# Kernel tuning notes

Measured on AMD Instinct MI355X. Metric: run time of the kernel, lower is better.

## Reference

```python
import jax, jax.numpy as jnp
import numpy as np

T = 4096          # total packed tokens
E = 1024          # embed_dim
H = 16            # num heads
D = E // H        # head_dim
NEG = -1e30       # masked score (fp32-safe; every row has >=1 valid key)


def setup_inputs() -> dict:
    key = jax.random.key(0)
    ks = jax.random.split(key, 10)
    hidden_states = jax.random.normal(ks[0], (T, E), dtype=jnp.float32)
    # ragged segment boundaries (8 segments, varying lengths, packed to T)
    cu_seqlens = jnp.array([0, 400, 900, 1500, 2100, 2600, 3100, 3700, T], dtype=jnp.int32)
    s = 0.02
    Wq = jax.random.normal(ks[1], (E, E), dtype=jnp.float32) * s
    bq = jax.random.normal(ks[2], (E,), dtype=jnp.float32) * s
    Wk = jax.random.normal(ks[3], (E, E), dtype=jnp.float32) * s
    bk = jax.random.normal(ks[4], (E,), dtype=jnp.float32) * s
    Wv = jax.random.normal(ks[5], (E, E), dtype=jnp.float32) * s
    bv = jax.random.normal(ks[6], (E,), dtype=jnp.float32) * s
    Wo = jax.random.normal(ks[7], (E, E), dtype=jnp.float32) * s
    bo = jax.random.normal(ks[8], (E,), dtype=jnp.float32) * s
    return {"hidden_states": hidden_states, "cu_seqlens": cu_seqlens,
            "Wq": Wq, "bq": bq, "Wk": Wk, "bk": bk,
            "Wv": Wv, "bv": bv, "Wo": Wo, "bo": bo}


def reference(hidden_states, cu_seqlens, Wq, bq, Wk, bk, Wv, bv, Wo, bo):
    dtype = hidden_states.dtype
    scale = D ** -0.5
    # projections (torch Linear: x @ W.T + b), split heads -> [T, H, D]
    q = (hidden_states @ Wq.T + bq).reshape(T, H, D)
    k = (hidden_states @ Wk.T + bk).reshape(T, H, D)
    v = (hidden_states @ Wv.T + bv).reshape(T, H, D)
    # segment id per token from cu_seqlens; block-diagonal (varlen) mask
    seg = jnp.searchsorted(cu_seqlens[1:], jnp.arange(T, dtype=cu_seqlens.dtype), side="right")
    same = seg[:, None] == seg[None, :]            # [T, T]
    scores = jnp.einsum("qhd,khd->hqk", q, k) * scale   # [H, T, T]
    scores = jnp.where(same[None], scores.astype(jnp.float32), NEG)
    attn = jax.nn.softmax(scores, axis=-1).astype(dtype)
    out = jnp.einsum("hqk,khd->qhd", attn, v).reshape(T, E)
    return out @ Wo.T + bo
```

## Files before the change

kernel.cpp:

```cpp
#include <hip/hip_runtime.h>
#include <stdint.h>

#define T_TOK 4096
#define E_DIM 1024
#define H_N   16
#define D_HD  64
#define NSEG  8

typedef unsigned short u16;
typedef uint32_t       u32;
typedef __bf16          bf16x8 __attribute__((ext_vector_type(8)));
typedef float           f32x4  __attribute__((ext_vector_type(4)));
typedef unsigned short  us8    __attribute__((ext_vector_type(8)));
typedef unsigned short  us4    __attribute__((ext_vector_type(4)));
typedef uint32_t        u32x4  __attribute__((ext_vector_type(4)));

__device__ __forceinline__ u16 f2bf(float f) {
  uint32_t u = __builtin_bit_cast(uint32_t, f);
  u += 0x7FFFu + ((u >> 16) & 1u);
  return (u16)(u >> 16);
}

__device__ __forceinline__ f32x4 mfma16(us8 a, us8 b, f32x4 c) {
  return __builtin_amdgcn_mfma_f32_16x16x32_bf16(
      __builtin_bit_cast(bf16x8, a), __builtin_bit_cast(bf16x8, b), c, 0, 0, 0);
}

__device__ __forceinline__ void async_load16(const void* g, void* l) {
  __builtin_amdgcn_global_load_lds(
      (const __attribute__((address_space(1))) void*)g,
      (__attribute__((address_space(3))) void*)l, 16, 0, 0);
}

__global__ __launch_bounds__(256) void cvt_all(
    const float* __restrict__ hs, const float* __restrict__ wq,
    const float* __restrict__ wk, const float* __restrict__ wv,
    const float* __restrict__ wo,
    u16* __restrict__ xb, u16* __restrict__ wqkv, u16* __restrict__ wob) {
  const int NH = T_TOK * E_DIM / 4;
  const int NW = E_DIM * E_DIM / 4;
  int i = blockIdx.x * 256 + threadIdx.x;
  const float4* src; u16* dst; size_t off;
  if (i < NH)            { src = (const float4*)hs; dst = xb;   off = i; }
  else if (i < NH+NW)    { src = (const float4*)wq; dst = wqkv; off = i - NH;          src += off; off += 0;      goto L; }
  else if (i < NH+2*NW)  { src = (const float4*)wk; dst = wqkv; off = i - NH - NW;     src += off; off += NW;     goto L; }
  else if (i < NH+3*NW)  { src = (const float4*)wv; dst = wqkv; off = i - NH - 2*NW;   src += off; off += 2*NW;   goto L; }
  else                   { src = (const float4*)wo; dst = wob;  off = i - NH - 3*NW;   src += off;                goto L; }
  src += off;
L:
  float4 v = *src;
  us4 o;
  o[0] = f2bf(v.x); o[1] = f2bf(v.y); o[2] = f2bf(v.z); o[3] = f2bf(v.w);
  *(us4*)(dst + off * 4) = o;
}

template <int MODE>
__global__ __launch_bounds__(256, 2) void gemm_bt(
    const u16* __restrict__ A, const u16* __restrict__ B,
    int M, int N, int K,
    const float* __restrict__ bias0, const float* __restrict__ bias1,
    const float* __restrict__ bias2,
    u16* __restrict__ out_q, u16* __restrict__ out_k, u16* __restrict__ out_v,
    float* __restrict__ out_f) {
  __shared__ u16 As[2][128 * 32];
  __shared__ u16 Bs[2][128 * 32];

  const int nbn = N / 128;
  int bm = blockIdx.x / nbn, bn = blockIdx.x % nbn;
  int m0 = bm * 128, n0 = bn * 128;
  int tid = threadIdx.x, lane = tid & 63, wave = tid >> 6;
  int wr = wave >> 1, wc = wave & 1;

  f32x4 acc[4][4] = {};

  auto stage = [&](int bufi, int k0) {
#pragma unroll
    for (int r = 0; r < 2; ++r) {
      int chunk = r * 4 + wave;
      int elem = chunk * 512 + lane * 8;
      int row = elem >> 5, kc = elem & 31;
      async_load16(A + (size_t)(m0 + row) * K + k0 + kc, (char*)As[bufi] + chunk * 1024);
      async_load16(B + (size_t)(n0 + row) * K + k0 + kc, (char*)Bs[bufi] + chunk * 1024);
    }
  };

  stage(0, 0);
  __syncthreads();
  int NT = K / 32;
  int lrow = lane & 15, lk = (lane >> 4) * 8;
  for (int t = 0; t < NT; ++t) {
    int buf = t & 1;
    if (t + 1 < NT) stage(buf ^ 1, (t + 1) * 32);
    us8 a[4], b[4];
#pragma unroll
    for (int i = 0; i < 4; ++i) {
      a[i] = *(const us8*)&As[buf][(wr * 64 + i * 16 + lrow) * 32 + lk];
      b[i] = *(const us8*)&Bs[buf][(wc * 64 + i * 16 + lrow) * 32 + lk];
    }
#pragma unroll
    for (int i = 0; i < 4; ++i)
#pragma unroll
      for (int j = 0; j < 4; ++j)
        acc[i][j] = mfma16(a[i], b[j], acc[i][j]);
    __syncthreads();
  }

  int lg = lane >> 4;
#pragma unroll
  for (int i = 0; i < 4; ++i) {
#pragma unroll
    for (int j = 0; j < 4; ++j) {
      int col = n0 + wc * 64 + j * 16 + lrow;
      int row0 = m0 + wr * 64 + i * 16 + lg * 4;
      if (MODE == 0) {
        if (col < 1024) {
          int hh = col >> 6, dd = col & 63;
          float bb = bias0[col];
          u16* dst = out_q + (size_t)hh * (T_TOK * D_HD) + dd;
#pragma unroll
          for (int r = 0; r < 4; ++r)
            dst[(size_t)(row0 + r) * D_HD] = f2bf(acc[i][j][r] + bb);
        } else if (col < 2048) {
          int c = col - 1024;
          int hh = c >> 6, dd = c & 63;
          float bb = bias1[c];
          u16* dst = out_k + (size_t)hh * (T_TOK * D_HD) + dd;
#pragma unroll
          for (int r = 0; r < 4; ++r)
            dst[(size_t)(row0 + r) * D_HD] = f2bf(acc[i][j][r] + bb);
        } else {
          int vc = col - 2048;
          float bb = bias2[vc];
          us4 o;
#pragma unroll
          for (int r = 0; r < 4; ++r) o[r] = f2bf(acc[i][j][r] + bb);
          *(us4*)&out_v[(size_t)vc * T_TOK + row0] = o;
        }
      } else {
        float bb = bias0[col];
#pragma unroll
        for (int r = 0; r < 4; ++r)
          out_f[(size_t)(row0 + r) * 1024 + col] = acc[i][j][r] + bb;
      }
    }
  }
}

__global__ __launch_bounds__(256, 4) void attn_varlen3(
    const u16* __restrict__ Qh, const u16* __restrict__ Kh,
    const u16* __restrict__ Vt, const int* __restrict__ cu,
    u16* __restrict__ Ctx) {
  __shared__ u16 Ks[2][64 * 64];
  __shared__ u16 Vs[2][64 * 64];

  int orig = blockIdx.x;
  int swz = (orig & 7) * 128 + (orig >> 3);
  int qt = swz & 63, h = swz >> 6;
  int tid = threadIdx.x, lane = tid & 63, wave = tid >> 6;
  int lrow = lane & 15, lg = lane >> 4;
  int q0b = qt * 64;
  int q = q0b + wave * 16 + lrow;

  int cuv[NSEG + 1];
#pragma unroll
  for (int i = 0; i <= NSEG; ++i) cuv[i] = cu[i];

  int s = 0, sl = 0, sh = 0;
#pragma unroll
  for (int i = 1; i < NSEG; ++i) {
    s  += (q >= cuv[i]);
    sl += (q0b >= cuv[i]);
    sh += (q0b + 63 >= cuv[i]);
  }
  int kb = cuv[s], ke = cuv[s + 1];
  int kt0 = cuv[sl] & ~7;
  int kend = cuv[sh + 1];
  int NT = (kend - kt0 + 63) >> 6;

  const u16* qp = Qh + ((size_t)h * T_TOK + q) * D_HD + lg * 8;
  us8 qB0 = *(const us8*)(qp);
  us8 qB1 = *(const us8*)(qp + 32);

  const u16* Kbase = Kh + (size_t)h * (T_TOK * D_HD);
  const u16* Vbase = Vt + (size_t)h * (D_HD * T_TOK);

  int c0 = wave * 2, c1 = wave * 2 + 1;
  int row0_ = c0 * 8 + (lane >> 3), row1_ = c1 * 8 + (lane >> 3);
  int g0 = (row0_ & 3) | (((row0_ >> 3) & 1) << 2);
  int g1 = (row1_ & 3) | (((row1_ >> 3) & 1) << 2);
  int ss0 = (lane & 7) ^ g0, ss1 = (lane & 7) ^ g1;

  auto stage = [&](int bufi, int ktn) {
    async_load16(Kbase + (size_t)(ktn + row0_) * D_HD + ss0 * 8,
                 (char*)Ks[bufi] + c0 * 1024);
    async_load16(Kbase + (size_t)(ktn + row1_) * D_HD + ss1 * 8,
                 (char*)Ks[bufi] + c1 * 1024);
    async_load16(Vbase + (size_t)row0_ * T_TOK + ktn + ss0 * 8,
                 (char*)Vs[bufi] + c0 * 1024);
    async_load16(Vbase + (size_t)row1_ * T_TOK + ktn + ss1 * 8,
                 (char*)Vs[bufi] + c1 * 1024);
  };

  const float scale2 = 0.125f * 1.44269504f;
  float mrun = -1e30f, lrun = 0.f;
  f32x4 accO[4] = {};

  stage(0, kt0);
  __syncthreads();

  for (int t = 0; t < NT; ++t) {
    int ktn = kt0 + t * 64;
    int buf = t & 1;
    if (t + 1 < NT) stage(buf ^ 1, ktn + 64);

    us8 kA[4][2];
#pragma unroll
    for (int f = 0; f < 4; ++f) {
      int krl = (f & 1) * 32 + (lrow >> 2) * 8 + (f >> 1) * 4 + (lrow & 3);
      int gk = (krl & 3) | (((krl >> 3) & 1) << 2);
      kA[f][0] = *(const us8*)((char*)Ks[buf] + krl * 128 + (lg ^ gk) * 16);
      kA[f][1] = *(const us8*)((char*)Ks[buf] + krl * 128 + ((lg | 4) ^ gk) * 16);
    }
    f32x4 s_[4];
#pragma unroll
    for (int f = 0; f < 4; ++f) {
      f32x4 z = {};
      z = mfma16(kA[f][0], qB0, z);
      s_[f] = mfma16(kA[f][1], qB1, z);
    }

    us8 vA[4][2];
#pragma unroll
    for (int nf = 0; nf < 4; ++nf) {
      int d_l = nf * 16 + lrow;
      int gv = (d_l & 3) | (((d_l >> 3) & 1) << 2);
#pragma unroll
      for (int ks = 0; ks < 2; ++ks)
        vA[nf][ks] = *(const us8*)((char*)Vs[buf] + d_l * 128 +
                                   (((ks << 2) | lg) ^ gv) * 16);
    }

    float mx = -1e30f;
#pragma unroll
    for (int f = 0; f < 4; ++f) {
      int kb0 = ktn + (f & 1) * 32 + lg * 8 + (f >> 1) * 4;
#pragma unroll
      for (int r = 0; r < 4; ++r) {
        int key = kb0 + r;
        float sv = (key >= kb && key < ke) ? s_[f][r] * scale2 : -1e30f;
        s_[f][r] = sv;
        mx = fmaxf(mx, sv);
      }
    }
    mx = fmaxf(mx, __shfl_xor(mx, 16));
    mx = fmaxf(mx, __shfl_xor(mx, 32));
    float mn = fmaxf(mrun, mx);
    float scf = exp2f(mrun - mn);
    mrun = mn;
    float ts = 0.f;
#pragma unroll
    for (int f = 0; f < 4; ++f)
#pragma unroll
      for (int r = 0; r < 4; ++r) {
        float p = exp2f(s_[f][r] - mn);
        s_[f][r] = p;
        ts += p;
      }
    lrun = lrun * scf + ts;
#pragma unroll
    for (int nf = 0; nf < 4; ++nf)
#pragma unroll
      for (int r = 0; r < 4; ++r) accO[nf][r] *= scf;

    u32 pw[8];
#pragma unroll
    for (int f = 0; f < 4; ++f)
#pragma unroll
      for (int pp = 0; pp < 2; ++pp)
        asm("v_cvt_pk_bf16_f32 %0, %1, %2"
            : "=v"(pw[f * 2 + pp])
            : "v"(s_[f][2 * pp]), "v"(s_[f][2 * pp + 1]));
    us8 pB0 = __builtin_bit_cast(us8, (u32x4){pw[0], pw[1], pw[4], pw[5]});
    us8 pB1 = __builtin_bit_cast(us8, (u32x4){pw[2], pw[3], pw[6], pw[7]});

#pragma unroll
    for (int nf = 0; nf < 4; ++nf) {
      accO[nf] = mfma16(vA[nf][0], pB0, accO[nf]);
      accO[nf] = mfma16(vA[nf][1], pB1, accO[nf]);
    }

    __syncthreads();
  }

  lrun += __shfl_xor(lrun, 16);
  lrun += __shfl_xor(lrun, 32);
  float inv = 1.f / lrun;
  u16* op = Ctx + (size_t)q * E_DIM + h * D_HD + lg * 4;
#pragma unroll
  for (int nf = 0; nf < 4; ++nf) {
    us4 o;
#pragma unroll
    for (int r = 0; r < 4; ++r) o[r] = f2bf(accO[nf][r] * inv);
    *(us4*)(op + nf * 16) = o;
  }
}

extern "C" void kernel_launch(void* const* d_in, const int* in_sizes, int n_in,
                              void* d_out, int out_size, void* d_ws, size_t ws_size,
                              hipStream_t stream) {
  const float* hs = (const float*)d_in[0];
  const int*   cu = (const int*)d_in[1];
  const float* Wq = (const float*)d_in[2];
  const float* bq = (const float*)d_in[3];
  const float* Wk = (const float*)d_in[4];
  const float* bk = (const float*)d_in[5];
  const float* Wv = (const float*)d_in[6];
  const float* bv = (const float*)d_in[7];
  const float* Wo = (const float*)d_in[8];
  const float* bo = (const float*)d_in[9];
  float* out = (float*)d_out;

  char* ws = (char*)d_ws;
  u16* Xb   = (u16*)(ws);
  u16* Wqkv = (u16*)(ws + 8ll * 1024 * 1024);
  u16* Wob  = (u16*)(ws + 14ll * 1024 * 1024);
  u16* Qh   = (u16*)(ws + 16ll * 1024 * 1024);
  u16* Kh   = (u16*)(ws + 24ll * 1024 * 1024);
  u16* Vt   = (u16*)(ws + 32ll * 1024 * 1024);
  u16* Ctx  = (u16*)(ws + 40ll * 1024 * 1024);

  cvt_all<<<8192, 256, 0, stream>>>(hs, Wq, Wk, Wv, Wo, Xb, Wqkv, Wob);
  gemm_bt<0><<<dim3(32 * 24), 256, 0, stream>>>(Xb, Wqkv, T_TOK, 3 * E_DIM, E_DIM,
                                                bq, bk, bv, Qh, Kh, Vt, nullptr);
  attn_varlen3<<<dim3(64 * 16), 256, 0, stream>>>(Qh, Kh, Vt, cu, Ctx);
  gemm_bt<1><<<dim3(32 * 8), 256, 0, stream>>>(Ctx, Wob, T_TOK, E_DIM, E_DIM,
                                               bo, nullptr, nullptr,
                                               nullptr, nullptr, nullptr, out);
}
```

Before: 195.6 us.

## Fold softmax scale into Q, load V directly, skip masking and lazy rescale

Folds the softmax scale and log2e factor into the Q projection epilogue so the attention kernel no longer multiplies scores. V fragments now come straight from global memory instead of being staged through LDS, which drops the V shared buffer. Masking is skipped for tiles lying fully inside the segment, and the running-max rescale is skipped when the new max exceeds the old by at most 12 in log2 units. MFMA sections are wrapped in s_setprio. Direct V global loads may add latency, and the lazy rescale changes the numeric bounds on the exponentials.

```diff
diff --git a/kernel.cpp b/kernel.cpp
--- a/kernel.cpp
+++ b/kernel.cpp
@@ -116,10 +116,11 @@
         if (col < 1024) {
           int hh = col >> 6, dd = col & 63;
           float bb = bias0[col];
+          const float qs = 0.18033688f;
           u16* dst = out_q + (size_t)hh * (T_TOK * D_HD) + dd;
 #pragma unroll
           for (int r = 0; r < 4; ++r)
-            dst[(size_t)(row0 + r) * D_HD] = f2bf(acc[i][j][r] + bb);
+            dst[(size_t)(row0 + r) * D_HD] = f2bf((acc[i][j][r] + bb) * qs);
         } else if (col < 2048) {
           int c = col - 1024;
           int hh = c >> 6, dd = c & 63;
@@ -146,12 +147,11 @@
   }
 }
 
-__global__ __launch_bounds__(256, 4) void attn_varlen3(
+__global__ __launch_bounds__(256, 4) void attn_varlen4(
     const u16* __restrict__ Qh, const u16* __restrict__ Kh,
     const u16* __restrict__ Vt, const int* __restrict__ cu,
     u16* __restrict__ Ctx) {
   __shared__ u16 Ks[2][64 * 64];
-  __shared__ u16 Vs[2][64 * 64];
 
   int orig = blockIdx.x;
   int swz = (orig & 7) * 128 + (orig >> 3);
@@ -182,7 +182,7 @@
   us8 qB1 = *(const us8*)(qp + 32);
 
   const u16* Kbase = Kh + (size_t)h * (T_TOK * D_HD);
-  const u16* Vbase = Vt + (size_t)h * (D_HD * T_TOK);
+  const u16* Vbase = Vt + (size_t)h * (D_HD * T_TOK) + (size_t)lrow * T_TOK;
 
   int c0 = wave * 2, c1 = wave * 2 + 1;
   int row0_ = c0 * 8 + (lane >> 3), row1_ = c1 * 8 + (lane >> 3);
@@ -190,28 +190,31 @@
   int g1 = (row1_ & 3) | (((row1_ >> 3) & 1) << 2);
   int ss0 = (lane & 7) ^ g0, ss1 = (lane & 7) ^ g1;
 
-  auto stage = [&](int bufi, int ktn) {
+  auto stageK = [&](int bufi, int ktn) {
     async_load16(Kbase + (size_t)(ktn + row0_) * D_HD + ss0 * 8,
                  (char*)Ks[bufi] + c0 * 1024);
     async_load16(Kbase + (size_t)(ktn + row1_) * D_HD + ss1 * 8,
                  (char*)Ks[bufi] + c1 * 1024);
-    async_load16(Vbase + (size_t)row0_ * T_TOK + ktn + ss0 * 8,
-                 (char*)Vs[bufi] + c0 * 1024);
-    async_load16(Vbase + (size_t)row1_ * T_TOK + ktn + ss1 * 8,
-                 (char*)Vs[bufi] + c1 * 1024);
   };
 
-  const float scale2 = 0.125f * 1.44269504f;
   float mrun = -1e30f, lrun = 0.f;
   f32x4 accO[4] = {};
 
-  stage(0, kt0);
+  stageK(0, kt0);
   __syncthreads();
 
   for (int t = 0; t < NT; ++t) {
     int ktn = kt0 + t * 64;
     int buf = t & 1;
-    if (t + 1 < NT) stage(buf ^ 1, ktn + 64);
+    if (t + 1 < NT) stageK(buf ^ 1, ktn + 64);
+
+    us8 vA[4][2];
+#pragma unroll
+    for (int nf = 0; nf < 4; ++nf)
+#pragma unroll
+      for (int ks = 0; ks < 2; ++ks)
+        vA[nf][ks] = *(const us8*)(Vbase + (size_t)(nf * 16) * T_TOK +
+                                   ktn + ks * 32 + lg * 8);
 
     us8 kA[4][2];
 #pragma unroll
@@ -222,55 +225,66 @@
       kA[f][1] = *(const us8*)((char*)Ks[buf] + krl * 128 + ((lg | 4) ^ gk) * 16);
     }
     f32x4 s_[4];
+    __builtin_amdgcn_s_setprio(1);
 #pragma unroll
     for (int f = 0; f < 4; ++f) {
       f32x4 z = {};
       z = mfma16(kA[f][0], qB0, z);
       s_[f] = mfma16(kA[f][1], qB1, z);
     }
-
-    us8 vA[4][2];
-#pragma unroll
-    for (int nf = 0; nf < 4; ++nf) {
-      int d_l = nf * 16 + lrow;
-      int gv = (d_l & 3) | (((d_l >> 3) & 1) << 2);
-#pragma unroll
-      for (int ks = 0; ks < 2; ++ks)
-        vA[nf][ks] = *(const us8*)((char*)Vs[buf] + d_l * 128 +
-                                   (((ks << 2) | lg) ^ gv) * 16);
-    }
-
-    float mx = -1e30f;
-#pragma unroll
-    for (int f = 0; f < 4; ++f) {
-      int kb0 = ktn + (f & 1) * 32 + lg * 8 + (f >> 1) * 4;
-#pragma unroll
-      for (int r = 0; r < 4; ++r) {
-        int key = kb0 + r;
-        float sv = (key >= kb && key < ke) ? s_[f][r] * scale2 : -1e30f;
-        s_[f][r] = sv;
-        mx = fmaxf(mx, sv);
+    __builtin_amdgcn_s_setprio(0);
+
+    bool interior = (ktn >= kb) && (ktn + 64 <= ke);
+    if (!__all(interior)) {
+#pragma unroll
+      for (int f = 0; f < 4; ++f) {
+        int kb0 = ktn + (f & 1) * 32 + lg * 8 + (f >> 1) * 4;
+#pragma unroll
+        for (int r = 0; r < 4; ++r) {
+          int key = kb0 + r;
+          s_[f][r] = (key >= kb && key < ke) ? s_[f][r] : -1e30f;
+        }
       }
     }
+
+    float mx = fmaxf(fmaxf(fmaxf(s_[0][0], s_[0][1]), s_[0][2]),
+                     fmaxf(fmaxf(s_[0][3], s_[1][0]), s_[1][1]));
+    mx = fmaxf(mx, fmaxf(fmaxf(s_[1][2], s_[1][3]), s_[2][0]));
+    mx = fmaxf(mx, fmaxf(fmaxf(s_[2][1], s_[2][2]), s_[2][3]));
+    mx = fmaxf(mx, fmaxf(fmaxf(s_[3][0], s_[3][1]), fmaxf(s_[3][2], s_[3][3])));
     mx = fmaxf(mx, __shfl_xor(mx, 16));
     mx = fmaxf(mx, __shfl_xor(mx, 32));
-    float mn = fmaxf(mrun, mx);
-    float scf = exp2f(mrun - mn);
-    mrun = mn;
-    float ts = 0.f;
-#pragma unroll
-    for (int f = 0; f < 4; ++f)
-#pragma unroll
-      for (int r = 0; r < 4; ++r) {
-        float p = exp2f(s_[f][r] - mn);
-        s_[f][r] = p;
-        ts += p;
-      }
-    lrun = lrun * scf + ts;
-#pragma unroll
-    for (int nf = 0; nf < 4; ++nf)
-#pragma unroll
-      for (int r = 0; r < 4; ++r) accO[nf][r] *= scf;
+
+    if (__all(mx - mrun <= 12.0f)) {
+      float ts = 0.f;
+#pragma unroll
+      for (int f = 0; f < 4; ++f)
+#pragma unroll
+        for (int r = 0; r < 4; ++r) {
+          float p = exp2f(s_[f][r] - mrun);
+          s_[f][r] = p;
+          ts += p;
+        }
+      lrun += ts;
+    } else {
+      float mn = fmaxf(mrun, mx);
+      float scf = exp2f(mrun - mn);
+      mrun = mn;
+      float ts = 0.f;
+#pragma unroll
+      for (int f = 0; f < 4; ++f)
+#pragma unroll
+        for (int r = 0; r < 4; ++r) {
+          float p = exp2f(s_[f][r] - mn);
+          s_[f][r] = p;
+          ts += p;
+        }
+      lrun = lrun * scf + ts;
+#pragma unroll
+      for (int nf = 0; nf < 4; ++nf)
+#pragma unroll
+        for (int r = 0; r < 4; ++r) accO[nf][r] *= scf;
+    }
 
     u32 pw[8];
 #pragma unroll
@@ -283,11 +297,13 @@
     us8 pB0 = __builtin_bit_cast(us8, (u32x4){pw[0], pw[1], pw[4], pw[5]});
     us8 pB1 = __builtin_bit_cast(us8, (u32x4){pw[2], pw[3], pw[6], pw[7]});
 
+    __builtin_amdgcn_s_setprio(1);
 #pragma unroll
     for (int nf = 0; nf < 4; ++nf) {
       accO[nf] = mfma16(vA[nf][0], pB0, accO[nf]);
       accO[nf] = mfma16(vA[nf][1], pB1, accO[nf]);
     }
+    __builtin_amdgcn_s_setprio(0);
 
     __syncthreads();
   }
@@ -332,7 +348,7 @@
   cvt_all<<<8192, 256, 0, stream>>>(hs, Wq, Wk, Wv, Wo, Xb, Wqkv, Wob);
   gemm_bt<0><<<dim3(32 * 24), 256, 0, stream>>>(Xb, Wqkv, T_TOK, 3 * E_DIM, E_DIM,
                                                 bq, bk, bv, Qh, Kh, Vt, nullptr);
-  attn_varlen3<<<dim3(64 * 16), 256, 0, stream>>>(Qh, Kh, Vt, cu, Ctx);
+  attn_varlen4<<<dim3(64 * 16), 256, 0, stream>>>(Qh, Kh, Vt, cu, Ctx);
   gemm_bt<1><<<dim3(32 * 8), 256, 0, stream>>>(Ctx, Wob, T_TOK, E_DIM, E_DIM,
                                                bo, nullptr, nullptr,
                                                nullptr, nullptr, nullptr, out);
```

Measured after the change: 227.6 us. +16.4%, slower.
